# Optimization experiments

Measured on AMD Instinct MI355X. Metric: run time of the kernel, lower is better.

Reference implementation:

```python
import jax, jax.numpy as jnp
import numpy as np

D = 1024
H = 16
HD = D // H
EPS = 1e-6


def rms_norm(x, w):
    # x: [..., hd]; compute in float32 like the torch module
    xf = x.astype(jnp.float32)
    rms = jnp.sqrt(jnp.mean(xf * xf, axis=-1, keepdims=True) + EPS)
    return (xf / rms * w.astype(jnp.float32)).astype(x.dtype)


def setup_inputs() -> dict:
    key = jax.random.key(0)
    ks = jax.random.split(key, 6)
    B, S = 2, 2048
    x = jax.random.normal(ks[0], (B, S, D), dtype=jnp.float32)
    Wqkv = jax.random.normal(ks[1], (3 * D, D), dtype=jnp.float32) * (1.0 / np.sqrt(D))
    bqkv = jax.random.normal(ks[2], (3 * D,), dtype=jnp.float32) * 0.02
    Wproj = jax.random.normal(ks[3], (D, D), dtype=jnp.float32) * (1.0 / np.sqrt(D))
    bproj = jax.random.normal(ks[4], (D,), dtype=jnp.float32) * 0.02
    qn_w = jnp.ones((HD,), dtype=jnp.float32)
    kn_w = jnp.ones((HD,), dtype=jnp.float32)
    return {"x": x, "Wqkv": Wqkv, "bqkv": bqkv, "Wproj": Wproj, "bproj": bproj,
            "qn_w": qn_w, "kn_w": kn_w}


def reference(x, Wqkv, bqkv, Wproj, bproj, qn_w, kn_w):
    B, S, _ = x.shape
    # QKV projection: torch Linear is x @ W.T + b
    qkv = x @ Wqkv.T + bqkv                     # [B, S, 3D]
    qkv = qkv.reshape(B, S, 3, H, HD)
    q, k, v = qkv[:, :, 0], qkv[:, :, 1], qkv[:, :, 2]   # each [B, S, H, hd]
    q = rms_norm(q, qn_w)
    k = rms_norm(k, kn_w)
    # move heads forward: [B, H, S, hd]
    q = q.transpose(0, 2, 1, 3)
    k = k.transpose(0, 2, 1, 3)
    v = v.transpose(0, 2, 1, 3)
    scale = 1.0 / np.sqrt(HD)
    scores = jnp.einsum('bhsd,bhtd->bhst', q, k) * scale   # [B, H, S, S] (math backend)
    attn = jax.nn.softmax(scores, axis=-1)
    out = jnp.einsum('bhst,bhtd->bhsd', attn, v)            # [B, H, S, hd]
    out = out.transpose(0, 2, 1, 3).reshape(B, S, D)
    return out @ Wproj.T + bproj
```

## Files before the change

kernel.cpp:

```cpp
#include <hip/hip_runtime.h>
#include <hip/hip_bf16.h>
#include <math.h>

#define D_MODEL 1024
#define NH 16
#define HD 64
#define SEQ 2048
#define BATCH 2
#define NTOK (BATCH*SEQ)

typedef short bf16x8 __attribute__((ext_vector_type(8)));
typedef short s4 __attribute__((ext_vector_type(4)));
typedef float f32x4 __attribute__((ext_vector_type(4)));
typedef unsigned short us4 __attribute__((ext_vector_type(4)));

#define MFMA(a,b,c) __builtin_amdgcn_mfma_f32_16x16x32_bf16(a,b,c,0,0,0)

union bfu { __hip_bfloat16 b; unsigned short u; };
__device__ __forceinline__ unsigned short f2b(float f){ bfu t; t.b = __float2bfloat16(f); return t.u; }
__device__ __forceinline__ float b2f(unsigned short u){ bfu t; t.u = u; return __bfloat162float(t.b); }
__device__ __forceinline__ unsigned short f2bf(float f){
    unsigned int u = __float_as_uint(f);
    u += 0x7FFFu + ((u >> 16) & 1u);
    return (unsigned short)(u >> 16);
}

__device__ __forceinline__ void g2l16(const unsigned short* g, unsigned short* l){
    __builtin_amdgcn_global_load_lds(
        (const __attribute__((address_space(1))) unsigned int*)g,
        (__attribute__((address_space(3))) unsigned int*)l, 16, 0, 0);
}

#define WAITVM(N) asm volatile("s_waitcnt vmcnt(" #N ")" ::: "memory")
#define RBAR do{ __builtin_amdgcn_s_barrier(); __builtin_amdgcn_sched_barrier(0); }while(0)

#define OFF_X   128L
#define OFF_WQ  (OFF_X  + 4194304L)
#define OFF_BQ  (OFF_WQ + 3145728L)
#define OFF_WP  (OFF_BQ + 3072L)
#define OFF_BP  (OFF_WP + 1048576L)
#define OFF_QN  (OFF_BP + 1024L)
#define OFF_KN  (OFF_QN + 64L)
#define OFF_Q   (OFF_KN + 64L)
#define OFF_K   (OFF_Q  + 4194304L)
#define OFF_V   (OFF_K  + 4194304L)
#define OFF_A   (OFF_V  + 4194304L)


__global__ __launch_bounds__(256) void detect_kernel(
    const unsigned int* __restrict__ xraw, int* __restrict__ cnt)
{
    int i = blockIdx.x*256 + threadIdx.x;
    uint4 v = ((const uint4*)xraw)[i];
    unsigned int w[4] = {v.x, v.y, v.z, v.w};
    int local = 0;
    #pragma unroll
    for (int j=0;j<4;j++){
        local += ((w[j] & 0x7F80u) >= 0x4800u);
        local += (((w[j]>>16) & 0x7F80u) >= 0x4800u);
    }
    if (local) atomicAdd(cnt, local);
}

__global__ __launch_bounds__(256) void convert_kernel(
    const void* __restrict__ x,  const void* __restrict__ wq,
    const void* __restrict__ bq, const void* __restrict__ wp,
    const void* __restrict__ bp, const void* __restrict__ qn,
    const void* __restrict__ kn, unsigned short* __restrict__ ws,
    const int* __restrict__ cntp)
{
    const int flag = (*cntp > 256);
    long i = (long)blockIdx.x*blockDim.x + threadIdx.x;
    const long stride = (long)gridDim.x*blockDim.x;
    const long NCH = 2098208L;
    for (; i < NCH; i += stride){
        long j = i; const void* src; long off;
        if (j < 1048576L)                  { src = x;  off = OFF_X;  }
        else if ((j -= 1048576L) < 786432L){ src = wq; off = OFF_WQ; }
        else if ((j -= 786432L)  < 768L)   { src = bq; off = OFF_BQ; }
        else if ((j -= 768L)     < 262144L){ src = wp; off = OFF_WP; }
        else if ((j -= 262144L)  < 256L)   { src = bp; off = OFF_BP; }
        else if ((j -= 256L)     < 16L)    { src = qn; off = OFF_QN; }
        else      { j -= 16L;                src = kn; off = OFF_KN; }
        us4 o;
        if (flag){
            float4 v = ((const float4*)src)[j];
            o.x = f2b(v.x); o.y = f2b(v.y); o.z = f2b(v.z); o.w = f2b(v.w);
        } else {
            o = ((const us4*)src)[j];
        }
        *(us4*)(ws + off + j*4) = o;
    }
}

__global__ __launch_bounds__(256) void qkv_kernel(
    const unsigned short* __restrict__ x,
    const unsigned short* __restrict__ Wqkv,
    const unsigned short* __restrict__ bqkv,
    const unsigned short* __restrict__ qn_w,
    const unsigned short* __restrict__ kn_w,
    unsigned short* __restrict__ qbuf,
    unsigned short* __restrict__ kbuf,
    unsigned short* __restrict__ vbuf)
{
    __shared__ __align__(16) unsigned short tA0[128*32];
    __shared__ __align__(16) unsigned short tA1[128*32];
    __shared__ __align__(16) unsigned short tB0[128*32];
    __shared__ __align__(16) unsigned short tB1[128*32];
    const int tid  = threadIdx.x;
    const int w    = tid >> 6, lane = tid & 63, quad = lane >> 4, c = lane & 15;
    const int m0 = blockIdx.y*128, n0 = blockIdx.x*128;
    const int am = (w>>1)*64, bn = (w&1)*64;
    const int kq = quad ^ ((c>>1)&3);

    f32x4 acc[4][4];
    for (int mi=0;mi<4;mi++) for (int ni=0;ni<4;ni++) acc[mi][ni] = {0.f,0.f,0.f,0.f};

    const int i0 = tid, i1 = tid + 256;
    const int r0 = i0>>2, cc0 = (i0&3) ^ ((r0>>1)&3);
    const int r1 = i1>>2, cc1 = (i1&3) ^ ((r1>>1)&3);
    const long gaA0 = (long)(m0 + r0)*D_MODEL + cc0*8;
    const long gaA1 = (long)(m0 + r1)*D_MODEL + cc1*8;
    const long gbB0 = (long)(n0 + r0)*D_MODEL + cc0*8;
    const long gbB1 = (long)(n0 + r1)*D_MODEL + cc1*8;

#define QKV_STAGE(BUFA, BUFB, T) do{ const int kk_ = (T)*32; \
    g2l16(x    + gaA0 + kk_, BUFA + i0*8); \
    g2l16(x    + gaA1 + kk_, BUFA + i1*8); \
    g2l16(Wqkv + gbB0 + kk_, BUFB + i0*8); \
    g2l16(Wqkv + gbB1 + kk_, BUFB + i1*8); \
    __builtin_amdgcn_sched_barrier(0); }while(0)

#define QKV_COMP(BUFA, BUFB) do{ \
    bf16x8 a_[4], b_[4]; \
    _Pragma("unroll") \
    for (int mi=0;mi<4;mi++) \
        a_[mi] = *(const bf16x8*)(BUFA + ((am + mi*16 + c)*4 + kq)*8); \
    _Pragma("unroll") \
    for (int ni=0;ni<4;ni++) \
        b_[ni] = *(const bf16x8*)(BUFB + ((bn + ni*16 + c)*4 + kq)*8); \
    _Pragma("unroll") \
    for (int mi=0;mi<4;mi++) \
        _Pragma("unroll") \
        for (int ni=0;ni<4;ni++) \
            acc[mi][ni] = MFMA(a_[mi], b_[ni], acc[mi][ni]); }while(0)

    QKV_STAGE(tA0, tB0, 0);
    QKV_STAGE(tA1, tB1, 1);

    for (int t=0; t<30; t+=2){
        WAITVM(4); RBAR;
        QKV_COMP(tA0, tB0);
        RBAR;
        QKV_STAGE(tA0, tB0, t+2);
        WAITVM(4); RBAR;
        QKV_COMP(tA1, tB1);
        RBAR;
        QKV_STAGE(tA1, tB1, t+3);
    }
    WAITVM(4); RBAR;
    QKV_COMP(tA0, tB0);
    WAITVM(0); RBAR;
    QKV_COMP(tA1, tB1);
#undef QKV_STAGE
#undef QKV_COMP

    const int nw = n0 + bn, mw = m0 + am;
    const int region = nw >> 10;
    const int h      = (nw & 1023) >> 6;
    float bias[4], wn[4];
    for (int ni=0;ni<4;ni++){
        bias[ni] = b2f(bqkv[nw + ni*16 + c]);
        wn[ni]   = 1.0f;
    }
    if (region==0) for (int ni=0;ni<4;ni++) wn[ni] = b2f(qn_w[ni*16+c]) * 0.18033688f;
    if (region==1) for (int ni=0;ni<4;ni++) wn[ni] = b2f(kn_w[ni*16+c]);

    for (int mi=0;mi<4;mi++){
        for (int ni=0;ni<4;ni++)
            for (int r=0;r<4;r++) acc[mi][ni][r] += bias[ni];

        float scale_r[4];
        if (region < 2){
            for (int r=0;r<4;r++){
                float ss = 0.f;
                for (int ni=0;ni<4;ni++){ float v2 = acc[mi][ni][r]; ss += v2*v2; }
                ss += __shfl_xor(ss, 1, 64);
                ss += __shfl_xor(ss, 2, 64);
                ss += __shfl_xor(ss, 4, 64);
                ss += __shfl_xor(ss, 8, 64);
                scale_r[r] = rsqrtf(ss*(1.0f/64.0f) + 1e-6f);
            }
        } else {
            for (int r=0;r<4;r++) scale_r[r] = 1.0f;
        }

        for (int r=0;r<4;r++){
            int m = mw + mi*16 + quad*4 + r;
            int bidx = m >> 11, s = m & 2047;
            long bb = (long)(bidx*NH + h)*SEQ*HD;
            if (region == 0){
                long base = bb + (long)s*HD;
                for (int ni=0;ni<4;ni++)
                    qbuf[base + ni*16 + c] = f2bf(acc[mi][ni][r] * scale_r[r] * wn[ni]);
            } else if (region == 1){
                long tb = bb + (long)(s>>6)*4096;
                for (int ni=0;ni<4;ni++){
                    int d = ni*16 + c;
                    long idx = tb + (long)((s&63)*8 + ((d>>3) ^ (s&7)))*8 + (d&7);
                    kbuf[idx] = f2bf(acc[mi][ni][r] * scale_r[r] * wn[ni]);
                }
            } else {
                long tb = bb + (long)(s>>6)*4096;
                int ch2  = (s>>4)&3;
                int fb   = ((s>>2)&3)*4;
                int mloc = s&3;
                for (int ni=0;ni<4;ni++){
                    int d = ni*16 + c;
                    int f = fb + (((d>>1) + ch2)&3);
                    long idx = tb + (long)d*64 + f*4 + mloc;
                    vbuf[idx] = f2bf(acc[mi][ni][r]);
                }
            }
        }
    }
}

__global__ __launch_bounds__(256, 4) void attn_kernel(
    const unsigned short* __restrict__ qbuf,
    const unsigned short* __restrict__ kts,
    const unsigned short* __restrict__ vts,
    unsigned short* __restrict__ abuf)
{
    const int tid = threadIdx.x, w = tid>>6, lane = tid&63, quad = lane>>4, c = lane&15;
    const int bh = blockIdx.y, qt = blockIdx.x;
    const unsigned short* qb = qbuf + (long)bh*SEQ*HD;
    const unsigned short* kb = kts + (long)bh*SEQ*HD;
    const unsigned short* vb = vts + (long)bh*SEQ*HD;
    const int qbase = qt*64 + w*16;
    const int cq = c & 7;

    __shared__ __align__(16) unsigned short KT0[4096];
    __shared__ __align__(16) unsigned short KT1[4096];
    __shared__ __align__(16) unsigned short VT0[4096];
    __shared__ __align__(16) unsigned short VT1[4096];

    bf16x8 aq[2];
    #pragma unroll
    for (int ks=0;ks<2;ks++)
        aq[ks] = *(const bf16x8*)(qb + (long)(qbase + c)*HD + ks*32 + quad*8);

    f32x4 o[4];
    #pragma unroll
    for (int nt=0;nt<4;nt++) o[nt] = {0.f,0.f,0.f,0.f};
    f32x4 l4 = {0.f,0.f,0.f,0.f};

#define STAGE2(SRC, DST) do{ \
    g2l16((SRC) + tid*8,        DST + tid*8); \
    g2l16((SRC) + 2048 + tid*8, DST + 2048 + tid*8); }while(0)

#define ATTN_TILE(KTB, VTB) do{ \
    bf16x8 kf_[4][2]; \
    _Pragma("unroll") \
    for (int mt=0;mt<4;mt++) \
        _Pragma("unroll") \
        for (int ks=0;ks<2;ks++) \
            kf_[mt][ks] = *(const bf16x8*)(KTB + ((mt*16+c)*8 + ((ks*4+quad)^cq))*8); \
    f32x4 z4_[4]; \
    _Pragma("unroll") \
    for (int mt=0;mt<4;mt++){ \
        f32x4 t_ = {0.f,0.f,0.f,0.f}; \
        t_ = MFMA(kf_[mt][0], aq[0], t_); \
        t_ = MFMA(kf_[mt][1], aq[1], t_); \
        z4_[mt] = t_; \
    } \
    unsigned int pk_[4][2]; \
    _Pragma("unroll") \
    for (int mt=0;mt<4;mt++){ \
        float p0 = __builtin_amdgcn_exp2f(z4_[mt][0]); \
        float p1 = __builtin_amdgcn_exp2f(z4_[mt][1]); \
        float p2 = __builtin_amdgcn_exp2f(z4_[mt][2]); \
        float p3 = __builtin_amdgcn_exp2f(z4_[mt][3]); \
        l4[0] += p0; l4[1] += p1; l4[2] += p2; l4[3] += p3; \
        pk_[mt][0] = __builtin_amdgcn_perm(__float_as_uint(p1), __float_as_uint(p0), 0x07060302u); \
        pk_[mt][1] = __builtin_amdgcn_perm(__float_as_uint(p3), __float_as_uint(p2), 0x07060302u); \
    } \
    _Pragma("unroll") \
    for (int ks=0;ks<2;ks++){ \
        union { unsigned int u[4]; bf16x8 v; } pB_; \
        pB_.u[0] = pk_[2*ks][0];   pB_.u[1] = pk_[2*ks][1]; \
        pB_.u[2] = pk_[2*ks+1][0]; pB_.u[3] = pk_[2*ks+1][1]; \
        _Pragma("unroll") \
        for (int nt=0;nt<4;nt++){ \
            const int dv_ = nt*16 + c; \
            const unsigned short* vbase_ = VTB + dv_*64; \
            int flo_ = quad*4 + (((dv_>>1) + ks*2    )&3); \
            int fhi_ = quad*4 + (((dv_>>1) + ks*2 + 1)&3); \
            uint2 lo_ = *(const uint2*)(vbase_ + flo_*4); \
            uint2 hi_ = *(const uint2*)(vbase_ + fhi_*4); \
            union { unsigned int u[4]; bf16x8 v; } vv_; \
            vv_.u[0]=lo_.x; vv_.u[1]=lo_.y; vv_.u[2]=hi_.x; vv_.u[3]=hi_.y; \
            o[nt] = MFMA(vv_.v, pB_.v, o[nt]); \
        } \
    } }while(0)

    STAGE2(kb, KT0); STAGE2(vb, VT0);
    __syncthreads();

    for (int kt2=0; kt2<SEQ/64; kt2+=2){
        STAGE2(kb + (kt2+1)*4096, KT1);
        STAGE2(vb + (kt2+1)*4096, VT1);
        ATTN_TILE(KT0, VT0);
        __syncthreads();
        if (kt2+2 < SEQ/64){
            STAGE2(kb + (kt2+2)*4096, KT0);
            STAGE2(vb + (kt2+2)*4096, VT0);
        }
        ATTN_TILE(KT1, VT1);
        __syncthreads();
    }
#undef STAGE2
#undef ATTN_TILE

    float l_loc = (l4[0]+l4[1]) + (l4[2]+l4[3]);
    l_loc += __shfl_xor(l_loc, 16, 64);
    l_loc += __shfl_xor(l_loc, 32, 64);
    float inv = 1.0f / l_loc;

    const int b = bh >> 4, h = bh & 15;
    long base = ((long)(b*SEQ + qbase + c)*NH + h)*HD;
    #pragma unroll
    for (int nt=0;nt<4;nt++){
        us4 pkd;
        #pragma unroll
        for (int r=0;r<4;r++) pkd[r] = f2bf(o[nt][r]*inv);
        *(us4*)(abuf + base + nt*16 + quad*4) = pkd;
    }
}

__global__ __launch_bounds__(256) void proj_kernel(
    const unsigned short* __restrict__ abuf,
    const unsigned short* __restrict__ Wp,
    const unsigned short* __restrict__ bp,
    void* __restrict__ outv,
    const int* __restrict__ cntp)
{
    __shared__ __align__(16) unsigned short tA0[128*32];
    __shared__ __align__(16) unsigned short tA1[128*32];
    __shared__ __align__(16) unsigned short tB0[64*32];
    __shared__ __align__(16) unsigned short tB1[64*32];
    const int tid  = threadIdx.x;
    const int w    = tid >> 6, lane = tid & 63, quad = lane >> 4, c = lane & 15;
    const int m0 = blockIdx.y*128, n0 = blockIdx.x*64;
    const int am = (w>>1)*64, bn = (w&1)*32;
    const int kq = quad ^ ((c>>1)&3);
    const int flag = (*cntp > 256);

    f32x4 acc[4][2];
    for (int mi=0;mi<4;mi++) for (int ni=0;ni<2;ni++) acc[mi][ni] = {0.f,0.f,0.f,0.f};

    const int i0 = tid, i1 = tid + 256;
    const int r0 = i0>>2, cc0 = (i0&3) ^ ((r0>>1)&3);
    const int r1 = i1>>2, cc1 = (i1&3) ^ ((r1>>1)&3);
    const long gaA0 = (long)(m0 + r0)*D_MODEL + cc0*8;
    const long gaA1 = (long)(m0 + r1)*D_MODEL + cc1*8;
    const long gbB0 = (long)(n0 + r0)*D_MODEL + cc0*8;

#define PROJ_STAGE(BUFA, BUFB, T) do{ const int kk_ = (T)*32; \
    g2l16(abuf + gaA0 + kk_, BUFA + i0*8); \
    g2l16(abuf + gaA1 + kk_, BUFA + i1*8); \
    g2l16(Wp   + gbB0 + kk_, BUFB + i0*8); \
    __builtin_amdgcn_sched_barrier(0); }while(0)

#define PROJ_COMP(BUFA, BUFB) do{ \
    bf16x8 a_[4], b_[2]; \
    _Pragma("unroll") \
    for (int mi=0;mi<4;mi++) \
        a_[mi] = *(const bf16x8*)(BUFA + ((am + mi*16 + c)*4 + kq)*8); \
    _Pragma("unroll") \
    for (int ni=0;ni<2;ni++) \
        b_[ni] = *(const bf16x8*)(BUFB + ((bn + ni*16 + c)*4 + kq)*8); \
    _Pragma("unroll") \
    for (int mi=0;mi<4;mi++) \
        _Pragma("unroll") \
        for (int ni=0;ni<2;ni++) \
            acc[mi][ni] = MFMA(a_[mi], b_[ni], acc[mi][ni]); }while(0)

    PROJ_STAGE(tA0, tB0, 0);
    PROJ_STAGE(tA1, tB1, 1);

    for (int t=0; t<30; t+=2){
        WAITVM(3); RBAR;
        PROJ_COMP(tA0, tB0);
        RBAR;
        PROJ_STAGE(tA0, tB0, t+2);
        WAITVM(3); RBAR;
        PROJ_COMP(tA1, tB1);
        RBAR;
        PROJ_STAGE(tA1, tB1, t+3);
    }
    WAITVM(3); RBAR;
    PROJ_COMP(tA0, tB0);
    WAITVM(0); RBAR;
    PROJ_COMP(tA1, tB1);
#undef PROJ_STAGE
#undef PROJ_COMP

    float bias[2];
    for (int ni=0;ni<2;ni++) bias[ni] = b2f(bp[n0 + bn + ni*16 + c]);

    for (int mi=0;mi<4;mi++)
        for (int r=0;r<4;r++){
            long m = m0 + am + mi*16 + quad*4 + r;
            for (int ni=0;ni<2;ni++){
                float val = acc[mi][ni][r] + bias[ni];
                long idx = m*D_MODEL + n0 + bn + ni*16 + c;
                if (flag) ((float*)outv)[idx] = val;
                else      ((unsigned short*)outv)[idx] = f2bf(val);
            }
        }
}

extern "C" void kernel_launch(void* const* d_in, const int* in_sizes, int n_in,
                              void* d_out, int out_size, void* d_ws, size_t ws_size,
                              hipStream_t stream)
{
    unsigned short* ws = (unsigned short*)d_ws;
    int* cnt = (int*)d_ws;

    hipMemsetAsync(cnt, 0, 4, stream);
    hipLaunchKernelGGL(detect_kernel, dim3(16), dim3(256), 0, stream,
                       (const unsigned int*)d_in[0], cnt);
    hipLaunchKernelGGL(convert_kernel, dim3(2048), dim3(256), 0, stream,
                       d_in[0], d_in[1], d_in[2], d_in[3], d_in[4], d_in[5], d_in[6],
                       ws, cnt);
    hipLaunchKernelGGL(qkv_kernel,  dim3(24,32), dim3(256), 0, stream,
                       ws+OFF_X, ws+OFF_WQ, ws+OFF_BQ, ws+OFF_QN, ws+OFF_KN,
                       ws+OFF_Q, ws+OFF_K, ws+OFF_V);
    hipLaunchKernelGGL(attn_kernel, dim3(32,32), dim3(256), 0, stream,
                       ws+OFF_Q, ws+OFF_K, ws+OFF_V, ws+OFF_A);
    hipLaunchKernelGGL(proj_kernel, dim3(16,32), dim3(256), 0, stream,
                       ws+OFF_A, ws+OFF_WP, ws+OFF_BP, d_out, cnt);
}
```

Measured before the change: 215.9 us.

## Switch attention K/V staging to vmcnt-gated pipeline, revert projection pipeline to syncthreads

The attention loop now issues K and V loads for two tiles ahead and gates each tile on a partial vmcnt wait plus a raw barrier, instead of full __syncthreads after every tile. This lets global-to-LDS loads for the next tile stay in flight while the current tile's MFMAs run. At the same time, the output projection GEMM drops its vmcnt-based pipeline and returns to a simple double-buffer with __syncthreads. The gain in attention depends on the WAITVM counts matching the number of outstanding loads, and the projection may lose some overlap.

```diff
diff --git a/kernel.cpp b/kernel.cpp
--- a/kernel.cpp
+++ b/kernel.cpp
@@ -255,9 +255,12 @@
     for (int nt=0;nt<4;nt++) o[nt] = {0.f,0.f,0.f,0.f};
     f32x4 l4 = {0.f,0.f,0.f,0.f};
 
-#define STAGE2(SRC, DST) do{ \
-    g2l16((SRC) + tid*8,        DST + tid*8); \
-    g2l16((SRC) + 2048 + tid*8, DST + 2048 + tid*8); }while(0)
+#define ASTAGE(KTB, VTB, T) do{ const long off_ = (long)(T)*4096; \
+    g2l16(kb + off_ + tid*8,        KTB + tid*8); \
+    g2l16(kb + off_ + 2048 + tid*8, KTB + 2048 + tid*8); \
+    g2l16(vb + off_ + tid*8,        VTB + tid*8); \
+    g2l16(vb + off_ + 2048 + tid*8, VTB + 2048 + tid*8); \
+    __builtin_amdgcn_sched_barrier(0); }while(0)
 
 #define ATTN_TILE(KTB, VTB) do{ \
     bf16x8 kf_[4][2]; \
@@ -304,22 +307,24 @@
         } \
     } }while(0)
 
-    STAGE2(kb, KT0); STAGE2(vb, VT0);
-    __syncthreads();
-
-    for (int kt2=0; kt2<SEQ/64; kt2+=2){
-        STAGE2(kb + (kt2+1)*4096, KT1);
-        STAGE2(vb + (kt2+1)*4096, VT1);
+    ASTAGE(KT0, VT0, 0);
+    ASTAGE(KT1, VT1, 1);
+
+    for (int kt2=0; kt2<30; kt2+=2){
+        WAITVM(4); RBAR;
         ATTN_TILE(KT0, VT0);
-        __syncthreads();
-        if (kt2+2 < SEQ/64){
-            STAGE2(kb + (kt2+2)*4096, KT0);
-            STAGE2(vb + (kt2+2)*4096, VT0);
-        }
+        RBAR;
+        ASTAGE(KT0, VT0, kt2+2);
+        WAITVM(4); RBAR;
         ATTN_TILE(KT1, VT1);
-        __syncthreads();
-    }
-#undef STAGE2
+        RBAR;
+        ASTAGE(KT1, VT1, kt2+3);
+    }
+    WAITVM(4); RBAR;
+    ATTN_TILE(KT0, VT0);
+    WAITVM(0); RBAR;
+    ATTN_TILE(KT1, VT1);
+#undef ASTAGE
 #undef ATTN_TILE
 
     float l_loc = (l4[0]+l4[1]) + (l4[2]+l4[3]);
@@ -369,8 +374,7 @@
 #define PROJ_STAGE(BUFA, BUFB, T) do{ const int kk_ = (T)*32; \
     g2l16(abuf + gaA0 + kk_, BUFA + i0*8); \
     g2l16(abuf + gaA1 + kk_, BUFA + i1*8); \
-    g2l16(Wp   + gbB0 + kk_, BUFB + i0*8); \
-    __builtin_amdgcn_sched_barrier(0); }while(0)
+    g2l16(Wp   + gbB0 + kk_, BUFB + i0*8); }while(0)
 
 #define PROJ_COMP(BUFA, BUFB) do{ \
     bf16x8 a_[4], b_[2]; \
@@ -387,22 +391,16 @@
             acc[mi][ni] = MFMA(a_[mi], b_[ni], acc[mi][ni]); }while(0)
 
     PROJ_STAGE(tA0, tB0, 0);
-    PROJ_STAGE(tA1, tB1, 1);
-
-    for (int t=0; t<30; t+=2){
-        WAITVM(3); RBAR;
+    __syncthreads();
+
+    for (int t=0; t<32; t+=2){
+        PROJ_STAGE(tA1, tB1, t+1);
         PROJ_COMP(tA0, tB0);
-        RBAR;
-        PROJ_STAGE(tA0, tB0, t+2);
-        WAITVM(3); RBAR;
+        __syncthreads();
+        if (t+2 < 32) PROJ_STAGE(tA0, tB0, t+2);
         PROJ_COMP(tA1, tB1);
-        RBAR;
-        PROJ_STAGE(tA1, tB1, t+3);
-    }
-    WAITVM(3); RBAR;
-    PROJ_COMP(tA0, tB0);
-    WAITVM(0); RBAR;
-    PROJ_COMP(tA1, tB1);
+        __syncthreads();
+    }
 #undef PROJ_STAGE
 #undef PROJ_COMP
 
```

Measured after the change: 238.0 us. 10.3% more time.
